# Performance work log

Measured on AMD Instinct MI355X. Metric: run time of the kernel, lower is better.

Reference implementation:

```python
import jax, jax.numpy as jnp
import numpy as np

NUM_HEADS = 12


def setup_inputs() -> dict:
    key = jax.random.key(0)
    ks = jax.random.split(key, 5)
    R, C, B, E = 256, 256, 1, 768
    s = 1.0 / np.sqrt(E)
    x = jax.random.normal(ks[0], (R, C, B, E), dtype=jnp.float32)
    Wq = jax.random.normal(ks[1], (E, E), dtype=jnp.float32) * s
    Wk = jax.random.normal(ks[2], (E, E), dtype=jnp.float32) * s
    Wv = jax.random.normal(ks[3], (E, E), dtype=jnp.float32) * s
    Wo = jax.random.normal(ks[4], (E, E), dtype=jnp.float32) * s
    z = jnp.zeros((E,), dtype=jnp.float32)
    return {"x": x, "Wq": Wq, "bq": z, "Wk": Wk, "bk": z,
            "Wv": Wv, "bv": z, "Wo": Wo, "bo": z}


def reference(x, Wq, bq, Wk, bk, Wv, bv, Wo, bo):
    R, C, B, E = x.shape
    H = NUM_HEADS
    Dh = E // H
    # align scaling: head_dim**-0.5 / sqrt(num_rows)
    scaling = (Dh ** -0.5) / jnp.sqrt(jnp.asarray(R, x.dtype))
    q = (x @ Wq.T + bq).reshape(R, C, B, H, Dh) * scaling
    k = (x @ Wk.T + bk).reshape(R, C, B, H, Dh)
    v = (x @ Wv.T + bv).reshape(R, C, B, H, Dh)
    # scores reduce over the row axis r BEFORE the shared softmax: [H,B,C,C]
    attn_weights = jnp.einsum('rinhd,rjnhd->hnij', q, k)
    attn_probs = jax.nn.softmax(attn_weights, axis=-1)  # dropout=0
    # shared probs applied to every row's values
    context = jnp.einsum('hnij,rjnhd->rinhd', attn_probs, v).reshape(R, C, B, E)
    output = context @ Wo.T + bo
    return (output, attn_probs)
```

## Files before the change

### kernel.cpp

```cpp
#include <hip/hip_runtime.h>
#include <cstdint>

typedef _Float16 f16;
typedef _Float16 f16x8 __attribute__((ext_vector_type(8)));
typedef float    f32x4 __attribute__((ext_vector_type(4)));

#define OFF_XH   0UL
#define OFF_QT   100663296UL
#define OFF_KT   201326592UL
#define OFF_VT   301989888UL
#define OFF_WQ   402653184UL
#define OFF_WK   403832832UL
#define OFF_WV   405012480UL
#define OFF_WO   406192128UL
#define OFF_PH   407371776UL

__global__ __launch_bounds__(256) void cast_f32_f16(const float* __restrict__ in,
                                                    f16* __restrict__ out, int n8) {
    int i = blockIdx.x * 256 + threadIdx.x;
    if (i >= n8) return;
    const float4* p = (const float4*)in;
    float4 a = p[2*i], b = p[2*i+1];
    f16x8 o;
    o[0]=(f16)a.x; o[1]=(f16)a.y; o[2]=(f16)a.z; o[3]=(f16)a.w;
    o[4]=(f16)b.x; o[5]=(f16)b.y; o[6]=(f16)b.z; o[7]=(f16)b.w;
    ((f16x8*)out)[i] = o;
}

enum { MODE_QK = 0, MODE_V = 1, MODE_SPLIT = 2, MODE_CTX = 3, MODE_OUT = 4 };

__device__ __forceinline__ void gl_lds16(const f16* g, f16* l) {
    auto gp = (const __attribute__((address_space(1))) f16*)(g);
    auto lp = (__attribute__((address_space(3))) f16*)(l);
    __builtin_amdgcn_global_load_lds(gp, lp, 16, 0, 0);
}

template<int MODE>
__global__ __launch_bounds__(256) void gemm_fast(
    const f16* __restrict__ A, const f16* __restrict__ B,
    float* __restrict__ outF, f16* __restrict__ outH,
    const float* __restrict__ bias, float scale,
    int lda, int ldb, int K)
{
    __shared__ f16 As[128*64];
    __shared__ f16 Bs[128*64];
    const int tid = threadIdx.x;
    const int wv = tid >> 6, ln = tid & 63;
    const int lrow = ln & 15, quad = ln >> 4;
    const int wm = wv >> 1, wn = wv & 1;
    const int m0 = blockIdx.y * 128;
    const int n0 = blockIdx.x * 128;
    const int z = blockIdx.z;
    int h = 0, sp = 0;
    if constexpr (MODE == MODE_SPLIT) {
        h = z >> 4; sp = z & 15;
        A += (long)h*4194304 + sp*1024;
        B += (long)h*4194304 + sp*1024;
    } else if constexpr (MODE == MODE_CTX) {
        A += (long)z * 65536;
        B += (long)z * 4194304;
    }

    const int srow = wv*32 + (ln >> 3);
    const int scol = ((ln & 7) ^ (srow & 7)) << 3;
    const f16* ga = A + (long)(m0 + srow)*lda + scol;
    const f16* gb = B + (long)(n0 + srow)*ldb + scol;

    f32x4 acc[4][4] = {};

    for (int k0 = 0; k0 < K; k0 += 64) {
        __syncthreads();
        #pragma unroll
        for (int t = 0; t < 4; t++) {
            gl_lds16(ga + (long)t*8*lda, As + (wv*4 + t)*512);
            gl_lds16(gb + (long)t*8*ldb, Bs + (wv*4 + t)*512);
        }
        ga += 64; gb += 64;
        __syncthreads();
        #pragma unroll
        for (int ks = 0; ks < 2; ks++) {
            const int slot = ((ks*4 + quad) ^ (lrow & 7)) << 3;
            f16x8 af[4], bf[4];
            #pragma unroll
            for (int i = 0; i < 4; i++)
                af[i] = *(const f16x8*)&As[(wm*64 + i*16 + lrow)*64 + slot];
            #pragma unroll
            for (int j = 0; j < 4; j++)
                bf[j] = *(const f16x8*)&Bs[(wn*64 + j*16 + lrow)*64 + slot];
            #pragma unroll
            for (int i = 0; i < 4; i++)
                #pragma unroll
                for (int j = 0; j < 4; j++)
                    acc[i][j] = __builtin_amdgcn_mfma_f32_16x16x32_f16(af[i], bf[j], acc[i][j], 0, 0, 0);
        }
    }

    #pragma unroll
    for (int i = 0; i < 4; i++) {
        #pragma unroll
        for (int j = 0; j < 4; j++) {
            #pragma unroll
            for (int r = 0; r < 4; r++) {
                int m = m0 + wm*64 + i*16 + quad*4 + r;
                int n = n0 + wn*64 + j*16 + lrow;
                float v = acc[i][j][r];
                if constexpr (MODE == MODE_QK) {
                    v = (v + bias[n]) * scale;
                    outH[(((long)((n>>6)*256 + (m&255))*256 + (m>>8))<<6) + (n&63)] = (f16)v;
                } else if constexpr (MODE == MODE_V) {
                    v = v + bias[n];
                    outH[(((long)((n>>6)*256 + (m>>8))*64 + (n&63))<<8) + (m&255)] = (f16)v;
                } else if constexpr (MODE == MODE_SPLIT) {
                    outF[(long)sp*786432 + h*65536 + m*256 + n] = v;
                } else if constexpr (MODE == MODE_CTX) {
                    outH[((long)((n>>6)*256 + m))*768 + z*64 + (n&63)] = (f16)v;
                } else {
                    outF[(long)m*768 + n] = v + bias[n];
                }
            }
        }
    }
}

__global__ __launch_bounds__(256) void softmax_k(const float* __restrict__ Sp,
                                                 float* __restrict__ pOut,
                                                 f16* __restrict__ Ph) {
    __shared__ float red[8];
    const int row = blockIdx.x;
    const int t = threadIdx.x;
    float v = 0.f;
    #pragma unroll
    for (int s = 0; s < 16; s++)
        v += Sp[(long)s*786432 + (long)row*256 + t];
    float mx = v;
    #pragma unroll
    for (int o = 32; o; o >>= 1) mx = fmaxf(mx, __shfl_xor(mx, o, 64));
    if ((t & 63) == 0) red[t >> 6] = mx;
    __syncthreads();
    mx = fmaxf(fmaxf(red[0], red[1]), fmaxf(red[2], red[3]));
    float e = expf(v - mx);
    float s = e;
    #pragma unroll
    for (int o = 32; o; o >>= 1) s += __shfl_xor(s, o, 64);
    if ((t & 63) == 0) red[4 + (t >> 6)] = s;
    __syncthreads();
    s = red[4] + red[5] + red[6] + red[7];
    float p = e / s;
    pOut[(long)row*256 + t] = p;
    Ph[(long)row*256 + t] = (f16)p;
}

extern "C" void kernel_launch(void* const* d_in, const int* in_sizes, int n_in,
                              void* d_out, int out_size, void* d_ws, size_t ws_size,
                              hipStream_t stream) {
    const float* x  = (const float*)d_in[0];
    const float* Wq = (const float*)d_in[1];
    const float* bq = (const float*)d_in[2];
    const float* Wk = (const float*)d_in[3];
    const float* bk = (const float*)d_in[4];
    const float* Wv = (const float*)d_in[5];
    const float* bv = (const float*)d_in[6];
    const float* Wo = (const float*)d_in[7];
    const float* bo = (const float*)d_in[8];
    float* out   = (float*)d_out;
    float* probs = out + 50331648L;

    char* ws = (char*)d_ws;
    f16*   Xh   = (f16*)(ws + OFF_XH);
    float* Sp   = (float*)(ws + OFF_XH);
    f16*   CTXh = (f16*)(ws + OFF_XH);
    f16*   Qt   = (f16*)(ws + OFF_QT);
    f16*   Kt   = (f16*)(ws + OFF_KT);
    f16*   Vt   = (f16*)(ws + OFF_VT);
    f16*   Wqh  = (f16*)(ws + OFF_WQ);
    f16*   Wkh  = (f16*)(ws + OFF_WK);
    f16*   Wvh  = (f16*)(ws + OFF_WV);
    f16*   Woh  = (f16*)(ws + OFF_WO);
    f16*   Ph   = (f16*)(ws + OFF_PH);

    cast_f32_f16<<<24576, 256, 0, stream>>>(x,  Xh,  6291456);
    cast_f32_f16<<<288,   256, 0, stream>>>(Wq, Wqh, 73728);
    cast_f32_f16<<<288,   256, 0, stream>>>(Wk, Wkh, 73728);
    cast_f32_f16<<<288,   256, 0, stream>>>(Wv, Wvh, 73728);
    cast_f32_f16<<<288,   256, 0, stream>>>(Wo, Woh, 73728);

    dim3 g1(6, 512, 1);
    gemm_fast<MODE_QK><<<g1, 256, 0, stream>>>(Xh, Wqh, nullptr, Qt, bq, 1.0f/128.0f, 768, 768, 768);
    gemm_fast<MODE_QK><<<g1, 256, 0, stream>>>(Xh, Wkh, nullptr, Kt, bk, 1.0f,        768, 768, 768);
    gemm_fast<MODE_V ><<<g1, 256, 0, stream>>>(Xh, Wvh, nullptr, Vt, bv, 1.0f,        768, 768, 768);

    gemm_fast<MODE_SPLIT><<<dim3(2, 2, 192), 256, 0, stream>>>(Qt, Kt, Sp, nullptr, nullptr, 1.0f, 16384, 16384, 1024);

    softmax_k<<<3072, 256, 0, stream>>>(Sp, probs, Ph);

    gemm_fast<MODE_CTX><<<dim3(128, 2, 12), 256, 0, stream>>>(Ph, Vt, nullptr, CTXh, nullptr, 1.0f, 256, 256, 256);

    gemm_fast<MODE_OUT><<<g1, 256, 0, stream>>>(CTXh, Woh, out, nullptr, bo, 1.0f, 768, 768, 768);
}
```

Measured before the change: 993.1 us.

## Add triple-buffered 256x128 GEMM kernel with async LDS prefetch for projections

Introduces a new GEMM kernel using 512 threads, 256x128 output tiles, and a three-stage LDS ring buffer. Global-to-LDS loads for tile t+2 are issued while MFMAs run on tile t, with explicit vmcnt waits, barriers and setprio. Block indices are swizzled for L2 locality. It is used for the Q/K/V projections, the context GEMM and the output GEMM, and is meant to hide memory latency and reduce per-iteration sync stalls. The cost is more LDS per block (about 144 KB), which limits occupancy, plus fragile hand-tuned waitcnt logic.

```diff
diff --git a/kernel.cpp b/kernel.cpp
--- a/kernel.cpp
+++ b/kernel.cpp
@@ -33,6 +33,12 @@
     auto gp = (const __attribute__((address_space(1))) f16*)(g);
     auto lp = (__attribute__((address_space(3))) f16*)(l);
     __builtin_amdgcn_global_load_lds(gp, lp, 16, 0, 0);
+}
+
+__device__ __forceinline__ f16x8 ds_read_b128_f16(unsigned off) {
+    f16x8 r;
+    asm volatile("ds_read_b128 %0, %1" : "=v"(r) : "v"(off));
+    return r;
 }
 
 template<int MODE>
@@ -122,6 +128,128 @@
     }
 }
 
+template<int MODE>
+__global__ __launch_bounds__(512, 2) void gemm3b(
+    const f16* __restrict__ A, const f16* __restrict__ B,
+    float* __restrict__ outF, f16* __restrict__ outH,
+    const float* __restrict__ bias, float scale,
+    int lda, int ldb, int K)
+{
+    __shared__ f16 As[3][16384];
+    __shared__ f16 Bs[3][8192];
+    const int tid = threadIdx.x;
+    const int wv = tid >> 6, ln = tid & 63;
+    const int lrow = ln & 15, quad = ln >> 4;
+    const int wm = wv >> 1, wn = wv & 1;
+
+    int bx, by, z = 0;
+    if constexpr (MODE == MODE_CTX) {
+        bx = blockIdx.x; by = 0; z = blockIdx.z;
+    } else {
+        int lin = blockIdx.x;
+        int swz = (lin & 7) * 192 + (lin >> 3);
+        bx = swz % 6; by = swz / 6;
+    }
+    const int m0 = by * 256, n0 = bx * 128;
+
+    const f16* Ab = A; const f16* Bb = B;
+    if constexpr (MODE == MODE_CTX) { Ab += (long)z*65536; Bb += (long)z*4194304; }
+
+    const int srow = tid >> 3;
+    const int scol = (((tid & 7) ^ (srow & 7)) << 3);
+    const f16* gA = Ab + (long)(m0 + srow)*lda + scol;
+    const f16* gB = Bb + (long)(n0 + srow)*ldb + scol;
+
+    typedef __attribute__((address_space(3))) f16 lds_f16;
+    const unsigned asBase = (unsigned)(uintptr_t)(lds_f16*)&As[0][0];
+    const unsigned bsBase = (unsigned)(uintptr_t)(lds_f16*)&Bs[0][0];
+
+    const int NT = K >> 6;
+
+    auto stageA = [&](int buf, int kOff, int iss) {
+        gl_lds16(gA + (long)iss*64*lda + kOff, &As[buf][iss*4096 + wv*512]);
+    };
+    auto stageB = [&](int buf, int kOff, int iss) {
+        gl_lds16(gB + (long)iss*64*ldb + kOff, &Bs[buf][iss*4096 + wv*512]);
+    };
+
+    #pragma unroll
+    for (int tt = 0; tt < 2; ++tt) {
+        stageA(tt, tt*64, 0); stageA(tt, tt*64, 1);
+        stageA(tt, tt*64, 2); stageA(tt, tt*64, 3);
+        stageB(tt, tt*64, 0); stageB(tt, tt*64, 1);
+    }
+    asm volatile("s_waitcnt vmcnt(6)" ::: "memory");
+    __builtin_amdgcn_sched_barrier(0);
+    __builtin_amdgcn_s_barrier();
+
+    f32x4 acc[4][4] = {};
+    int buf = 0;
+    for (int t = 0; t < NT; ++t) {
+        const int sb = (buf >= 1) ? buf - 1 : buf + 2;
+        const bool doStage = (t + 2) < NT;
+        const int kOff = (t + 2) << 6;
+        const unsigned aB = asBase + (unsigned)buf * 32768u;
+        const unsigned bB = bsBase + (unsigned)buf * 16384u;
+        #pragma unroll
+        for (int ph = 0; ph < 2; ++ph) {
+            const unsigned slotB = (unsigned)(((ph*4 + quad) ^ (lrow & 7)) << 4);
+            f16x8 af[4], bf[4];
+            #pragma unroll
+            for (int i = 0; i < 4; ++i)
+                af[i] = ds_read_b128_f16(aB + ((unsigned)(wm*64 + i*16 + lrow) << 7) + slotB);
+            #pragma unroll
+            for (int j = 0; j < 4; ++j)
+                bf[j] = ds_read_b128_f16(bB + ((unsigned)(wn*64 + j*16 + lrow) << 7) + slotB);
+            if (doStage) {
+                if (ph == 0) { stageA(sb, kOff, 0); stageA(sb, kOff, 1); stageB(sb, kOff, 0); }
+                else         { stageA(sb, kOff, 2); stageA(sb, kOff, 3); stageB(sb, kOff, 1); }
+            }
+            __builtin_amdgcn_s_barrier();
+            asm volatile("s_waitcnt lgkmcnt(0)" ::: "memory");
+            __builtin_amdgcn_sched_barrier(0);
+            __builtin_amdgcn_s_setprio(1);
+            #pragma unroll
+            for (int i = 0; i < 4; ++i)
+                #pragma unroll
+                for (int j = 0; j < 4; ++j)
+                    acc[i][j] = __builtin_amdgcn_mfma_f32_16x16x32_f16(af[i], bf[j], acc[i][j], 0, 0, 0);
+            __builtin_amdgcn_s_setprio(0);
+            if (ph == 1 && t < NT - 1) {
+                if (t <= NT - 3) asm volatile("s_waitcnt vmcnt(6)" ::: "memory");
+                else             asm volatile("s_waitcnt vmcnt(0)" ::: "memory");
+                __builtin_amdgcn_sched_barrier(0);
+            }
+            __builtin_amdgcn_s_barrier();
+        }
+        buf = (buf == 2) ? 0 : buf + 1;
+    }
+
+    #pragma unroll
+    for (int i = 0; i < 4; ++i) {
+        #pragma unroll
+        for (int j = 0; j < 4; ++j) {
+            #pragma unroll
+            for (int r = 0; r < 4; ++r) {
+                int m = m0 + wm*64 + i*16 + quad*4 + r;
+                int n = n0 + wn*64 + j*16 + lrow;
+                float v = acc[i][j][r];
+                if constexpr (MODE == MODE_QK) {
+                    v = (v + bias[n]) * scale;
+                    outH[(((long)((n>>6)*256 + (m&255))*256 + (m>>8))<<6) + (n&63)] = (f16)v;
+                } else if constexpr (MODE == MODE_V) {
+                    v = v + bias[n];
+                    outH[(((long)((n>>6)*256 + (m>>8))*64 + (n&63))<<8) + (m&255)] = (f16)v;
+                } else if constexpr (MODE == MODE_CTX) {
+                    outH[((long)((n>>6)*256 + m))*768 + z*64 + (n&63)] = (f16)v;
+                } else {
+                    outF[(long)m*768 + n] = v + bias[n];
+                }
+            }
+        }
+    }
+}
+
 __global__ __launch_bounds__(256) void softmax_k(const float* __restrict__ Sp,
                                                  float* __restrict__ pOut,
                                                  f16* __restrict__ Ph) {
@@ -184,16 +312,15 @@
     cast_f32_f16<<<288,   256, 0, stream>>>(Wv, Wvh, 73728);
     cast_f32_f16<<<288,   256, 0, stream>>>(Wo, Woh, 73728);
 
-    dim3 g1(6, 512, 1);
-    gemm_fast<MODE_QK><<<g1, 256, 0, stream>>>(Xh, Wqh, nullptr, Qt, bq, 1.0f/128.0f, 768, 768, 768);
-    gemm_fast<MODE_QK><<<g1, 256, 0, stream>>>(Xh, Wkh, nullptr, Kt, bk, 1.0f,        768, 768, 768);
-    gemm_fast<MODE_V ><<<g1, 256, 0, stream>>>(Xh, Wvh, nullptr, Vt, bv, 1.0f,        768, 768, 768);
+    gemm3b<MODE_QK><<<1536, 512, 0, stream>>>(Xh, Wqh, nullptr, Qt, bq, 1.0f/128.0f, 768, 768, 768);
+    gemm3b<MODE_QK><<<1536, 512, 0, stream>>>(Xh, Wkh, nullptr, Kt, bk, 1.0f,        768, 768, 768);
+    gemm3b<MODE_V ><<<1536, 512, 0, stream>>>(Xh, Wvh, nullptr, Vt, bv, 1.0f,        768, 768, 768);
 
     gemm_fast<MODE_SPLIT><<<dim3(2, 2, 192), 256, 0, stream>>>(Qt, Kt, Sp, nullptr, nullptr, 1.0f, 16384, 16384, 1024);
 
     softmax_k<<<3072, 256, 0, stream>>>(Sp, probs, Ph);
 
-    gemm_fast<MODE_CTX><<<dim3(128, 2, 12), 256, 0, stream>>>(Ph, Vt, nullptr, CTXh, nullptr, 1.0f, 256, 256, 256);
-
-    gemm_fast<MODE_OUT><<<g1, 256, 0, stream>>>(CTXh, Woh, out, nullptr, bo, 1.0f, 768, 768, 768);
-}
+    gemm3b<MODE_CTX><<<dim3(128, 1, 12), 512, 0, stream>>>(Ph, Vt, nullptr, CTXh, nullptr, 1.0f, 256, 256, 256);
+
+    gemm3b<MODE_OUT><<<1536, 512, 0, stream>>>(CTXh, Woh, out, nullptr, bo, 1.0f, 768, 768, 768);
+}
```

Measured after the change: 953.8 us. 4.0% less time.
